# Kernel optimization log

Hardware: AMD Instinct MI355X
Metric: run time of the kernel (lower is better)

## Reference

```python
import jax, jax.numpy as jnp
import numpy as np

N, E = 50000, 300000
IN, FC, AC, H, C1, C2, OUT = 1024, 128, 20, 4, 10, 5, 3
FCN = FC + AC + H * C2  # 168


def bn_eval(x, g, b):
    # BatchNorm1d in eval mode with running_mean=0, running_var=1
    return x * (g / jnp.sqrt(1.0 + 1e-5)) + b


def add_self_loops(edge_index, edge_attr, n):
    # PyG add_self_loops with fill_value='mean': self-loop attr = mean of incoming edge attrs
    src, dst = edge_index[0], edge_index[1]
    ones = jnp.ones(src.shape[0], jnp.float32)
    deg = jax.ops.segment_sum(ones, dst, num_segments=n)
    mean_attr = jax.ops.segment_sum(edge_attr, dst, num_segments=n) / jnp.maximum(deg, 1.0)[:, None]
    loop = jnp.arange(n, dtype=src.dtype)
    return (jnp.concatenate([src, loop]), jnp.concatenate([dst, loop]),
            jnp.concatenate([edge_attr, mean_attr], 0))


def gatv2(x, src, dst, eattr, Wl, bl, Wr, br, We, att, b, n):
    # GATv2Conv (concat=True, negative_slope=0.2, edge_dim=1)
    h, c = att.shape
    xl = (x @ Wl + bl).reshape(n, h, c)
    xr = (x @ Wr + br).reshape(n, h, c)
    em = (eattr @ We).reshape(-1, h, c)
    m = jax.nn.leaky_relu(xl[src] + xr[dst] + em, 0.2)   # [E', H, C]
    logit = jnp.einsum('ehc,hc->eh', m, att)              # [E', H]
    mx = jax.ops.segment_max(logit, dst, num_segments=n)
    ex = jnp.exp(logit - mx[dst])
    den = jax.ops.segment_sum(ex, dst, num_segments=n)
    alpha = ex / (den[dst] + 1e-16)                       # segment softmax over dst
    out = jax.ops.segment_sum(xl[src] * alpha[..., None], dst, num_segments=n)
    return out.reshape(n, h * c) + b


def setup_inputs() -> dict:
    key = jax.random.key(0)
    ks = jax.random.split(key, 24)
    rn = lambda k, s: jax.random.normal(k, s, jnp.float32) * 0.05
    return {
        'features': jax.random.normal(ks[0], (N, IN), jnp.float32),
        'edges': jax.random.randint(ks[1], (2, E), 0, N),
        'edges2': jax.random.randint(ks[2], (2, E), 0, N),
        'edge_features': jax.random.normal(ks[3], (E, 1), jnp.float32),
        'additional_features': jax.random.normal(ks[4], (N, AC), jnp.float32),
        'sage_Wl': rn(ks[5], (IN, FC)), 'sage_bl': jnp.zeros((FC,), jnp.float32),
        'sage_Wr': rn(ks[6], (IN, FC)),
        'g1_Wl': rn(ks[7], (AC, H * C1)), 'g1_bl': jnp.zeros((H * C1,), jnp.float32),
        'g1_Wr': rn(ks[8], (AC, H * C1)), 'g1_br': jnp.zeros((H * C1,), jnp.float32),
        'g1_We': rn(ks[9], (1, H * C1)), 'g1_att': rn(ks[10], (H, C1)),
        'g1_b': jnp.zeros((H * C1,), jnp.float32),
        'g2_Wl': rn(ks[11], (H * C1, H * C2)), 'g2_bl': jnp.zeros((H * C2,), jnp.float32),
        'g2_Wr': rn(ks[12], (H * C1, H * C2)), 'g2_br': jnp.zeros((H * C2,), jnp.float32),
        'g2_We': rn(ks[13], (1, H * C2)), 'g2_att': rn(ks[14], (H, C2)),
        'g2_b': jnp.zeros((H * C2,), jnp.float32),
        'fc1_W': rn(ks[15], (FCN, FCN)), 'fc1_b': jnp.zeros((FCN,), jnp.float32),
        'fc2_W': rn(ks[16], (FCN, OUT)), 'fc2_b': jnp.zeros((OUT,), jnp.float32),
        'bnx_g': jnp.ones((FC,), jnp.float32), 'bnx_b': jnp.zeros((FC,), jnp.float32),
        'bny_g': jnp.ones((H * C2,), jnp.float32), 'bny_b': jnp.zeros((H * C2,), jnp.float32),
        'bnf_g': jnp.ones((FCN,), jnp.float32), 'bnf_b': jnp.zeros((FCN,), jnp.float32),
    }


def reference(features, edges, edges2, edge_features, additional_features,
              sage_Wl, sage_bl, sage_Wr,
              g1_Wl, g1_bl, g1_Wr, g1_br, g1_We, g1_att, g1_b,
              g2_Wl, g2_bl, g2_Wr, g2_br, g2_We, g2_att, g2_b,
              fc1_W, fc1_b, fc2_W, fc2_b,
              bnx_g, bnx_b, bny_g, bny_b, bnf_g, bnf_b):
    n = features.shape[0]
    # --- SAGEConv (mean aggr): out = lin_l(mean_j x_j) + lin_r(x_i) ---
    src, dst = edges[0], edges[1]
    deg = jax.ops.segment_sum(jnp.ones(src.shape[0], jnp.float32), dst, num_segments=n)
    aggr = jax.ops.segment_sum(features[src], dst, num_segments=n) / jnp.maximum(deg, 1.0)[:, None]
    x = aggr @ sage_Wl + sage_bl + features @ sage_Wr
    x = bn_eval(x, bnx_g, bnx_b)
    # --- GATv2 stack (self loops with mean edge-attr fill) ---
    s2, d2, ea = add_self_loops(edges2, edge_features, n)
    y = gatv2(additional_features, s2, d2, ea, g1_Wl, g1_bl, g1_Wr, g1_br, g1_We, g1_att, g1_b, n)
    y = jax.nn.leaky_relu(y, 0.01)  # activation (dropout off in eval)
    y = gatv2(y, s2, d2, ea, g2_Wl, g2_bl, g2_Wr, g2_br, g2_We, g2_att, g2_b, n)
    y = bn_eval(y, bny_g, bny_b)
    # --- MLP head ---
    z = jax.nn.leaky_relu(jnp.concatenate([x, y], axis=1), 0.01)
    z = jnp.concatenate([z, additional_features], axis=1) @ fc1_W + fc1_b
    z = jax.nn.relu(bn_eval(z, bnf_g, bnf_b))
    return z @ fc2_W + fc2_b
```

## Files before the change

### kernel.cpp

```cpp
#include <hip/hip_runtime.h>
#include <hip/hip_bf16.h>
#include <cfloat>

__device__ __forceinline__ float lrelu(float x, float a) { return x > 0.0f ? x : a * x; }

__device__ __forceinline__ unsigned short f2bf(float f) {
    unsigned u = __float_as_uint(f);
    unsigned r = (u + 0x7FFFu + ((u >> 16) & 1u)) >> 16;
    return (unsigned short)r;
}
__device__ __forceinline__ float bf2f(unsigned short u) {
    return __uint_as_float((unsigned)u << 16);
}

typedef __attribute__((ext_vector_type(8))) short short8;
typedef __attribute__((ext_vector_type(4))) float f32x4;

#define BN_RSQ 0.99999500003749968750f
#define SCAN_B 256
#define BAR_LGKM() asm volatile("s_waitcnt lgkmcnt(0)\n\ts_barrier" ::: "memory")

__global__ void zero_ws(uint4* __restrict__ p, int n16)
{
    int t = blockIdx.x * blockDim.x + threadIdx.x;
    if (t < n16) p[t] = make_uint4(0u, 0u, 0u, 0u);
}

__global__ void prep_all(const float* __restrict__ sWl, const float* __restrict__ sWr,
                         unsigned short* __restrict__ Btp,
                         const float* __restrict__ fc1W, unsigned short* __restrict__ Bt1p,
                         const float* __restrict__ g1Wl, const float* __restrict__ g1Wr,
                         unsigned short* __restrict__ Bg1,
                         const float* __restrict__ g2Wl, const float* __restrict__ g2Wr,
                         unsigned short* __restrict__ Bg2,
                         const int* __restrict__ e1d, const int* __restrict__ e2d,
                         const float* __restrict__ ef,
                         int* __restrict__ cnt1, int* __restrict__ cnt2,
                         float* __restrict__ easum, int E)
{
    int idx = blockIdx.x * blockDim.x + threadIdx.x;
    if (idx < 262144) {
        int j = idx & 7, lane = (idx >> 3) & 63, fn = (idx >> 9) & 3, wid = (idx >> 11) & 3, t = idx >> 13;
        int c = wid * 64 + fn * 16 + (lane & 15);
        int k = t * 32 + (lane >> 4) * 8 + j;
        float v = (c < 128) ? sWl[(size_t)k * 128 + c] : sWr[(size_t)k * 128 + (c - 128)];
        Btp[idx] = f2bf(v);
        return;
    }
    idx -= 262144;
    if (idx < 36864) {
        int j = idx & 7, lane = (idx >> 3) & 63, fn = (idx >> 9) & 3, q = idx >> 11;
        int wid = q % 3, t = q / 3;
        int c = wid * 64 + fn * 16 + (lane & 15);
        int k = t * 32 + (lane >> 4) * 8 + j;
        float v = (c < 168 && k < 168) ? fc1W[(size_t)k * 168 + c] : 0.0f;
        Bt1p[idx] = f2bf(v);
        return;
    }
    idx -= 36864;
    if (idx < 2560) {
        int j = idx & 7, lane = (idx >> 3) & 63, fn = idx >> 9;
        int c = fn * 16 + (lane & 15);
        int k = (lane >> 4) * 8 + j;
        float v = 0.0f;
        if (k < 20) v = (c < 40) ? g1Wl[(size_t)k * 40 + c] : g1Wr[(size_t)k * 40 + (c - 40)];
        Bg1[idx] = f2bf(v);
        return;
    }
    idx -= 2560;
    if (idx < 3072) {
        int j = idx & 7, lane = (idx >> 3) & 63, q = idx >> 9;
        int fn = q % 3, t = q / 3;
        int c = fn * 16 + (lane & 15);
        int k = t * 32 + (lane >> 4) * 8 + j;
        float v = 0.0f;
        if (k < 40 && c < 40) v = (c < 20) ? g2Wl[(size_t)k * 20 + c] : g2Wr[(size_t)k * 20 + (c - 20)];
        Bg2[idx] = f2bf(v);
        return;
    }
    idx -= 3072;
    if (idx < E) {
        atomicAdd(&cnt1[e1d[idx]], 1);
        int d2 = e2d[idx];
        atomicAdd(&cnt2[d2], 1);
        atomicAdd(&easum[d2], ef[idx]);
    }
}

__global__ void scan1(const int* __restrict__ cnt1, const int* __restrict__ cnt2,
                      int* __restrict__ off1, int* __restrict__ off2,
                      int* __restrict__ bsum1, int* __restrict__ bsum2, int M)
{
    __shared__ int sh[SCAN_B];
    int y = blockIdx.y;
    const int* cnt = y ? cnt2 : cnt1;
    int* excl = y ? off2 : off1;
    int* bsum = y ? bsum2 : bsum1;
    int i = blockIdx.x * SCAN_B + threadIdx.x;
    int v = (i < M) ? cnt[i] + y : 0;
    sh[threadIdx.x] = v;
    __syncthreads();
    for (int o = 1; o < SCAN_B; o <<= 1) {
        int t = (threadIdx.x >= o) ? sh[threadIdx.x - o] : 0;
        __syncthreads();
        sh[threadIdx.x] += t;
        __syncthreads();
    }
    if (i < M) excl[i] = sh[threadIdx.x] - v;
    if (threadIdx.x == SCAN_B - 1) bsum[blockIdx.x] = sh[threadIdx.x];
}

__global__ void scan2(int* __restrict__ bsum1, int* __restrict__ bsum2, int nb)
{
    __shared__ int sh[SCAN_B];
    int* bsum = blockIdx.y ? bsum2 : bsum1;
    int v = ((int)threadIdx.x < nb) ? bsum[threadIdx.x] : 0;
    sh[threadIdx.x] = v;
    __syncthreads();
    for (int o = 1; o < SCAN_B; o <<= 1) {
        int t = (threadIdx.x >= o) ? sh[threadIdx.x - o] : 0;
        __syncthreads();
        sh[threadIdx.x] += t;
        __syncthreads();
    }
    if ((int)threadIdx.x < nb) bsum[threadIdx.x] = sh[threadIdx.x] - v;
}

__global__ void scan3(int* __restrict__ off1, int* __restrict__ off2,
                      const int* __restrict__ bsum1, const int* __restrict__ bsum2,
                      const int* __restrict__ cnt1, const int* __restrict__ cnt2,
                      const float* __restrict__ easum, float* __restrict__ ealoop, int M)
{
    int y = blockIdx.y;
    int* off = y ? off2 : off1;
    const int* bsum = y ? bsum2 : bsum1;
    const int* cnt = y ? cnt2 : cnt1;
    int i = blockIdx.x * SCAN_B + threadIdx.x;
    if (i < M) {
        int v = off[i] + bsum[blockIdx.x];
        off[i] = v;
        if (i == M - 1) off[M] = v + cnt[i] + y;
        if (y) ealoop[i] = easum[i] / fmaxf((float)cnt2[i], 1.0f);
    }
}

__global__ __launch_bounds__(256) void stageA(
    const float* __restrict__ A, const unsigned short* __restrict__ Btp,
    unsigned short* __restrict__ P,
    const int* __restrict__ e1s, const int* __restrict__ e1d,
    const int* __restrict__ e2s, const int* __restrict__ e2d,
    const float* __restrict__ ef, const float* __restrict__ ealoop,
    const int* __restrict__ off1, const int* __restrict__ off2,
    int* __restrict__ cnt1, int* __restrict__ cnt2,
    int* __restrict__ srcs1, int2* __restrict__ se2,
    const float* __restrict__ addf, const unsigned short* __restrict__ Bg1,
    const float* __restrict__ g1bl, const float* __restrict__ g1br,
    unsigned short* __restrict__ xl1b, unsigned short* __restrict__ xr1b,
    int M, int E, int Eext, int Gg, int Gf)
{
    __shared__ __align__(16) char smem[20480];
    const int bid = blockIdx.x;
    const int tid = threadIdx.x;

    if (bid < Gg) {
        typedef unsigned short As2_t[64][72];
        As2_t* As2 = reinterpret_cast<As2_t*>(smem);
        const int wid = tid >> 6, lane = tid & 63;
        const int m0 = bid * 64;
        const int l16 = lane & 15, g = lane >> 4;
        const int colbase = wid * 64 + l16;
        const short8* Bv = reinterpret_cast<const short8*>(Btp);
        const int srow = tid >> 4, scol = (tid & 15) * 4;

        f32x4 acc[4][4] = {};
        float4 rcur[4], rnext[4];

#pragma unroll
        for (int p = 0; p < 4; ++p) {
            int ar = m0 + p * 16 + srow;
            rcur[p] = make_float4(0.f, 0.f, 0.f, 0.f);
            if (ar < M) rcur[p] = *reinterpret_cast<const float4*>(&A[(size_t)ar * 1024 + scol]);
        }
#pragma unroll
        for (int p = 0; p < 4; ++p) {
            ushort4 u;
            u.x = f2bf(rcur[p].x); u.y = f2bf(rcur[p].y); u.z = f2bf(rcur[p].z); u.w = f2bf(rcur[p].w);
            *reinterpret_cast<ushort4*>(&As2[0][p * 16 + srow][scol]) = u;
        }
#pragma unroll
        for (int p = 0; p < 4; ++p) {
            int ar = m0 + p * 16 + srow;
            rcur[p] = make_float4(0.f, 0.f, 0.f, 0.f);
            if (ar < M) rcur[p] = *reinterpret_cast<const float4*>(&A[(size_t)ar * 1024 + 64 + scol]);
        }
        BAR_LGKM();

        for (int c = 0; c < 16; ++c) {
            const int buf = c & 1;
            short8 bfr[2][4];
#pragma unroll
            for (int t = 0; t < 2; ++t)
#pragma unroll
                for (int fn = 0; fn < 4; ++fn)
                    bfr[t][fn] = Bv[(((c * 2 + t) * 4 + wid) * 4 + fn) * 64 + lane];
            if (c < 14) {
                const int k0 = (c + 2) * 64;
#pragma unroll
                for (int p = 0; p < 4; ++p) {
                    int ar = m0 + p * 16 + srow;
                    rnext[p] = make_float4(0.f, 0.f, 0.f, 0.f);
                    if (ar < M) rnext[p] = *reinterpret_cast<const float4*>(&A[(size_t)ar * 1024 + k0 + scol]);
                }
            }
#pragma unroll
            for (int t = 0; t < 2; ++t) {
                short8 afr[4];
#pragma unroll
                for (int fm = 0; fm < 4; ++fm)
                    afr[fm] = *reinterpret_cast<const short8*>(&As2[buf][fm * 16 + l16][t * 32 + g * 8]);
#pragma unroll
                for (int fm = 0; fm < 4; ++fm)
#pragma unroll
                    for (int fn = 0; fn < 4; ++fn)
                        acc[fm][fn] = __builtin_amdgcn_mfma_f32_16x16x32_bf16(
                            afr[fm], bfr[t][fn], acc[fm][fn], 0, 0, 0);
            }
            if (c < 15) {
#pragma unroll
                for (int p = 0; p < 4; ++p) {
                    ushort4 u;
                    u.x = f2bf(rcur[p].x); u.y = f2bf(rcur[p].y);
                    u.z = f2bf(rcur[p].z); u.w = f2bf(rcur[p].w);
                    *reinterpret_cast<ushort4*>(&As2[buf ^ 1][p * 16 + srow][scol]) = u;
                }
            }
            BAR_LGKM();
#pragma unroll
            for (int p = 0; p < 4; ++p) rcur[p] = rnext[p];
        }

#pragma unroll
        for (int fm = 0; fm < 4; ++fm) {
#pragma unroll
            for (int r = 0; r < 4; ++r) {
                int row = m0 + fm * 16 + g * 4 + r;
                if (row < M) {
#pragma unroll
                    for (int fn = 0; fn < 4; ++fn)
                        P[(size_t)row * 256 + colbase + fn * 16] = f2bf(acc[fm][fn][r]);
                }
            }
        }
    } else if (bid < Gg + Gf) {
        int t = (bid - Gg) * 256 + tid;
        if (t < E) {
            int d = e1d[t];
            int pos = atomicSub(&cnt1[d], 1) - 1;
            srcs1[off1[d] + pos] = e1s[t];
        }
        int t2 = t - E;
        if (t2 >= 0 && t2 < Eext) {
            if (t2 < E) {
                int d = e2d[t2];
                int pos = atomicSub(&cnt2[d], 1) - 1;
                se2[off2[d] + pos] = make_int2(e2s[t2], __float_as_int(ef[t2]));
            } else {
                int nn = t2 - E;
                se2[off2[nn + 1] - 1] = make_int2(nn, __float_as_int(ealoop[nn]));
            }
        }
    } else {
        const int wid = tid >> 6, lane = tid & 63;
        const int tile = (bid - Gg - Gf) * 4 + wid;
        const int m0 = tile * 64;
        if (m0 >= M) return;
        unsigned short (*xs)[40] = reinterpret_cast<unsigned short(*)[40]>(smem + wid * 5120);
        const int l16 = lane & 15, g = lane >> 4;
        const short8* Bv = reinterpret_cast<const short8*>(Bg1);

#pragma unroll
        for (int i = 0; i < 5; ++i) {
            int q = i * 64 + lane;
            int f = q * 4;
            int row = f / 20, col = f % 20;
            int ar = m0 + row;
            float4 v = make_float4(0.f, 0.f, 0.f, 0.f);
            if (ar < M) v = *reinterpret_cast<const float4*>(&addf[(size_t)ar * 20 + col]);
            ushort4 u;
            u.x = f2bf(v.x); u.y = f2bf(v.y); u.z = f2bf(v.z); u.w = f2bf(v.w);
            *reinterpret_cast<ushort4*>(&xs[row][col]) = u;
        }
        ushort4 zz; zz.x = 0; zz.y = 0; zz.z = 0; zz.w = 0;
#pragma unroll
        for (int c = 20; c < 32; c += 4)
            *reinterpret_cast<ushort4*>(&xs[lane][c]) = zz;

        f32x4 acc[4][5] = {};
        short8 afr[4], bfr[5];
#pragma unroll
        for (int fm = 0; fm < 4; ++fm)
            afr[fm] = *reinterpret_cast<const short8*>(&xs[fm * 16 + l16][g * 8]);
#pragma unroll
        for (int fn = 0; fn < 5; ++fn)
            bfr[fn] = Bv[fn * 64 + lane];
#pragma unroll
        for (int fm = 0; fm < 4; ++fm)
#pragma unroll
            for (int fn = 0; fn < 5; ++fn)
                acc[fm][fn] = __builtin_amdgcn_mfma_f32_16x16x32_bf16(
                    afr[fm], bfr[fn], acc[fm][fn], 0, 0, 0);

#pragma unroll
        for (int fm = 0; fm < 4; ++fm) {
#pragma unroll
            for (int r = 0; r < 4; ++r) {
                int row = m0 + fm * 16 + g * 4 + r;
                if (row < M) {
#pragma unroll
                    for (int fn = 0; fn < 5; ++fn) {
                        int col = fn * 16 + l16;
                        float v = acc[fm][fn][r];
                        if (col < 40) {
                            int h = col / 10, c = col % 10;
                            xl1b[((size_t)row * 4 + h) * 16 + c] = f2bf(v + g1bl[col]);
                        } else if (col < 80) {
                            int cc = col - 40, h = cc / 10, c = cc % 10;
                            xr1b[((size_t)row * 4 + h) * 16 + c] = f2bf(v + g1br[cc]);
                        }
                    }
                }
            }
        }
    }
}

template <int H, int C, int BPAD>
__device__ __forceinline__ void gat_node_compute(
    const int2* __restrict__ se2, const int* __restrict__ off2,
    const unsigned short* __restrict__ xlb, const unsigned short* __restrict__ xrb,
    const float* __restrict__ We, const float* __restrict__ att,
    int n, int h, float* __restrict__ outc)
{
    float xrc[C], atth[C], weh[C];
    {
        short8 sv[BPAD / 8];
#pragma unroll
        for (int q = 0; q < BPAD / 8; ++q)
            sv[q] = *reinterpret_cast<const short8*>(&xrb[((size_t)n * H + h) * BPAD + q * 8]);
#pragma unroll
        for (int c = 0; c < C; ++c) xrc[c] = bf2f((unsigned short)sv[c / 8][c % 8]);
    }
#pragma unroll
    for (int c = 0; c < C; ++c) {
        atth[c] = att[h * C + c];
        weh[c]  = We[h * C + c];
    }

    const int beg = off2[n], end = off2[n + 1];
    float mx = -FLT_MAX, den = 0.0f;
    float accv[C] = {};
    for (int j = beg; j < end; ++j) {
        int2 se = se2[j];
        int s = se.x;
        float ea = __int_as_float(se.y);
        short8 sv[BPAD / 8];
#pragma unroll
        for (int q = 0; q < BPAD / 8; ++q)
            sv[q] = *reinterpret_cast<const short8*>(&xlb[((size_t)s * H + h) * BPAD + q * 8]);
        float xv[C];
        float lg = 0.0f;
#pragma unroll
        for (int c = 0; c < C; ++c) {
            xv[c] = bf2f((unsigned short)sv[c / 8][c % 8]);
            float m = xv[c] + xrc[c] + ea * weh[c];
            lg += lrelu(m, 0.2f) * atth[c];
        }
        if (lg > mx) {
            float sc = __expf(mx - lg);
            den *= sc;
#pragma unroll
            for (int c = 0; c < C; ++c) accv[c] *= sc;
            mx = lg;
        }
        float ex = __expf(lg - mx);
        den += ex;
#pragma unroll
        for (int c = 0; c < C; ++c) accv[c] += ex * xv[c];
    }
    float inv = 1.0f / (den + 1e-16f);
#pragma unroll
    for (int c = 0; c < C; ++c) outc[c] = accv[c] * inv;
}

__global__ void stageB(const int* __restrict__ srcs1, const int* __restrict__ off1,
                       const unsigned short* __restrict__ P, const float* __restrict__ bl,
                       const float* __restrict__ bng, const float* __restrict__ bnb,
                       unsigned short* __restrict__ z128,
                       const int2* __restrict__ se2, const int* __restrict__ off2,
                       const unsigned short* __restrict__ xl1b, const unsigned short* __restrict__ xr1b,
                       const float* __restrict__ g1We, const float* __restrict__ g1att,
                       const float* __restrict__ g1b, float* __restrict__ y1,
                       int N, int Gg)
{
    const int bid = blockIdx.x;
    if (bid < Gg) {
        int t = bid * 256 + threadIdx.x;
        if (t >= N * 16) return;
        int n = t >> 4, g = t & 15;
        int beg = off1[n], end = off1[n + 1];
        float a[8] = {};
        for (int j = beg; j < end; ++j) {
            int s = srcs1[j];
            short8 v = *reinterpret_cast<const short8*>(&P[(size_t)s * 256 + g * 8]);
#pragma unroll
            for (int k = 0; k < 8; ++k) a[k] += bf2f((unsigned short)v[k]);
        }
        float inv = 1.0f / fmaxf((float)(end - beg), 1.0f);
        short8 pr = *reinterpret_cast<const short8*>(&P[(size_t)n * 256 + 128 + g * 8]);
        short8 zo;
#pragma unroll
        for (int k = 0; k < 8; ++k) {
            int cc = g * 8 + k;
            float x = a[k] * inv + bl[cc] + bf2f((unsigned short)pr[k]);
            x = x * (bng[cc] * BN_RSQ) + bnb[cc];
            zo[k] = (short)f2bf(lrelu(x, 0.01f));
        }
        *reinterpret_cast<short8*>(&z128[(size_t)n * 128 + g * 8]) = zo;
    } else {
        int t = (bid - Gg) * 256 + threadIdx.x;
        if (t >= N * 4) return;
        int n = t >> 2, h = t & 3;
        float oc[10];
        gat_node_compute<4, 10, 16>(se2, off2, xl1b, xr1b, g1We, g1att, n, h, oc);
#pragma unroll
        for (int c = 0; c < 10; ++c) {
            int jch = h * 10 + c;
            y1[(size_t)n * 40 + jch] = lrelu(oc[c] + g1b[jch], 0.01f);
        }
    }
}

__global__ __launch_bounds__(64) void gat_lin2_mfma(
    const float* __restrict__ X, const unsigned short* __restrict__ Bp,
    const float* __restrict__ bl, const float* __restrict__ br,
    unsigned short* __restrict__ xlb, unsigned short* __restrict__ xrb, int M)
{
    __shared__ unsigned short xs[64][72];
    const int lane = threadIdx.x;
    const int m0 = blockIdx.x * 64;
    const int l16 = lane & 15, g = lane >> 4;
    const short8* Bv = reinterpret_cast<const short8*>(Bp);

#pragma unroll
    for (int i = 0; i < 10; ++i) {
        int q = i * 64 + lane;
        int f = q * 4;
        int row = f / 40, col = f % 40;
        int ar = m0 + row;
        float4 v = make_float4(0.f, 0.f, 0.f, 0.f);
        if (ar < M) v = *reinterpret_cast<const float4*>(&X[(size_t)ar * 40 + col]);
        ushort4 u;
        u.x = f2bf(v.x); u.y = f2bf(v.y); u.z = f2bf(v.z); u.w = f2bf(v.w);
        *reinterpret_cast<ushort4*>(&xs[row][col]) = u;
    }
    ushort4 zz; zz.x = 0; zz.y = 0; zz.z = 0; zz.w = 0;
#pragma unroll
    for (int c = 40; c < 64; c += 4)
        *reinterpret_cast<ushort4*>(&xs[lane][c]) = zz;

    f32x4 acc[4][3] = {};
#pragma unroll
    for (int t = 0; t < 2; ++t) {
        short8 afr[4], bfr[3];
#pragma unroll
        for (int fm = 0; fm < 4; ++fm)
            afr[fm] = *reinterpret_cast<const short8*>(&xs[fm * 16 + l16][t * 32 + g * 8]);
#pragma unroll
        for (int fn = 0; fn < 3; ++fn)
            bfr[fn] = Bv[(t * 3 + fn) * 64 + lane];
#pragma unroll
        for (int fm = 0; fm < 4; ++fm)
#pragma unroll
            for (int fn = 0; fn < 3; ++fn)
                acc[fm][fn] = __builtin_amdgcn_mfma_f32_16x16x32_bf16(
                    afr[fm], bfr[fn], acc[fm][fn], 0, 0, 0);
    }

#pragma unroll
    for (int fm = 0; fm < 4; ++fm) {
#pragma unroll
        for (int r = 0; r < 4; ++r) {
            int row = m0 + fm * 16 + g * 4 + r;
            if (row < M) {
#pragma unroll
                for (int fn = 0; fn < 3; ++fn) {
                    int col = fn * 16 + l16;
                    float v = acc[fm][fn][r];
                    if (col < 20) {
                        int h = col / 5, c = col % 5;
                        xlb[((size_t)row * 4 + h) * 8 + c] = f2bf(v + bl[col]);
                    } else if (col < 40) {
                        int cc = col - 20, h = cc / 5, c = cc % 5;
                        xrb[((size_t)row * 4 + h) * 8 + c] = f2bf(v + br[cc]);
                    }
                }
            }
        }
    }
}

__global__ __launch_bounds__(256) void mlp_mfma(
    const unsigned short* __restrict__ z128, const float* __restrict__ addf,
    const int2* __restrict__ se2, const int* __restrict__ off2,
    const unsigned short* __restrict__ xl2b, const unsigned short* __restrict__ xr2b,
    const float* __restrict__ g2We, const float* __restrict__ g2att,
    const float* __restrict__ g2b,
    const float* __restrict__ bnyg, const float* __restrict__ bnyb,
    const unsigned short* __restrict__ Bt1p,
    const float* __restrict__ fc1b, const float* __restrict__ bnfg, const float* __restrict__ bnfb,
    const float* __restrict__ fc2W, const float* __restrict__ fc2b,
    float* __restrict__ out, int M)
{
    __shared__ __align__(16) char smem[64 * 169 * 4];
    unsigned short (*zs)[200] = reinterpret_cast<unsigned short(*)[200]>(smem);
    float (*ts)[169] = reinterpret_cast<float(*)[169]>(smem);
    const int tid = threadIdx.x;
    const int wid = tid >> 6, lane = tid & 63;
    const int m0 = blockIdx.x * 64;
    const int l16 = lane & 15, g = lane >> 4;
    const short8* Bv = reinterpret_cast<const short8*>(Bt1p);

    {
        int row = tid >> 2, h = tid & 3;
        int n = m0 + row;
        if (n < M) {
            float oc[5];
            gat_node_compute<4, 5, 8>(se2, off2, xl2b, xr2b, g2We, g2att, n, h, oc);
#pragma unroll
            for (int c = 0; c < 5; ++c) {
                int jch = h * 5 + c;
                float v = oc[c] + g2b[jch];
                v = v * (bnyg[jch] * BN_RSQ) + bnyb[jch];
                zs[row][128 + jch] = f2bf(lrelu(v, 0.01f));
            }
        } else {
#pragma unroll
            for (int c = 0; c < 5; ++c) zs[row][128 + h * 5 + c] = 0;
        }
    }

#pragma unroll
    for (int p = 0; p < 13; ++p) {
        int idx = p * 256 + tid;
        if (idx < 3200) {
            int row = idx / 50, c4 = (idx % 50) * 4;
            if (c4 >= 128 && c4 < 148) continue;
            int ar = m0 + row;
            ushort4 u; u.x = 0; u.y = 0; u.z = 0; u.w = 0;
            if (ar < M) {
                if (c4 < 128) {
                    u = *reinterpret_cast<const ushort4*>(&z128[(size_t)ar * 128 + c4]);
                } else if (c4 >= 148 && c4 < 168) {
                    float4 v = *reinterpret_cast<const float4*>(&addf[(size_t)ar * 20 + (c4 - 148)]);
                    u.x = f2bf(v.x); u.y = f2bf(v.y); u.z = f2bf(v.z); u.w = f2bf(v.w);
                }
            }
            *reinterpret_cast<ushort4*>(&zs[row][c4]) = u;
        }
    }
    __syncthreads();

    f32x4 acc[4][4] = {};
    if (wid < 3) {
#pragma unroll
        for (int t = 0; t < 6; ++t) {
            short8 afr[4], bfr[4];
#pragma unroll
            for (int fm = 0; fm < 4; ++fm)
                afr[fm] = *reinterpret_cast<const short8*>(&zs[fm * 16 + l16][t * 32 + g * 8]);
#pragma unroll
            for (int fn = 0; fn < 4; ++fn)
                bfr[fn] = Bv[((t * 3 + wid) * 4 + fn) * 64 + lane];
#pragma unroll
            for (int fm = 0; fm < 4; ++fm)
#pragma unroll
                for (int fn = 0; fn < 4; ++fn)
                    acc[fm][fn] = __builtin_amdgcn_mfma_f32_16x16x32_bf16(
                        afr[fm], bfr[fn], acc[fm][fn], 0, 0, 0);
        }
    }
    __syncthreads();
    if (wid < 3) {
        const int colbase = wid * 64 + l16;
#pragma unroll
        for (int fm = 0; fm < 4; ++fm) {
#pragma unroll
            for (int r = 0; r < 4; ++r) {
                int rr = fm * 16 + g * 4 + r;
#pragma unroll
                for (int fn = 0; fn < 4; ++fn) {
                    int col = colbase + fn * 16;
                    if (col < 168) {
                        float v = acc[fm][fn][r] + fc1b[col];
                        v = v * (bnfg[col] * BN_RSQ) + bnfb[col];
                        ts[rr][col] = fmaxf(v, 0.0f);
                    }
                }
            }
        }
    }
    __syncthreads();
    if (tid < 192) {
        int r = tid & 63, c = tid >> 6;
        float acc2 = fc2b[c];
#pragma unroll 4
        for (int k = 0; k < 168; ++k) acc2 += ts[r][k] * fc2W[k * 3 + c];
        int row = m0 + r;
        if (row < M) out[(size_t)row * 3 + c] = acc2;
    }
}

extern "C" void kernel_launch(void* const* d_in, const int* in_sizes, int n_in,
                              void* d_out, int out_size, void* d_ws, size_t ws_size,
                              hipStream_t stream)
{
    const float* features = (const float*)d_in[0];
    const int*   e1       = (const int*)d_in[1];
    const int*   e2       = (const int*)d_in[2];
    const float* ef       = (const float*)d_in[3];
    const float* addf     = (const float*)d_in[4];
    const float* sage_Wl  = (const float*)d_in[5];
    const float* sage_bl  = (const float*)d_in[6];
    const float* sage_Wr  = (const float*)d_in[7];
    const float* g1_Wl = (const float*)d_in[8];
    const float* g1_bl = (const float*)d_in[9];
    const float* g1_Wr = (const float*)d_in[10];
    const float* g1_br = (const float*)d_in[11];
    const float* g1_We = (const float*)d_in[12];
    const float* g1_att = (const float*)d_in[13];
    const float* g1_b = (const float*)d_in[14];
    const float* g2_Wl = (const float*)d_in[15];
    const float* g2_bl = (const float*)d_in[16];
    const float* g2_Wr = (const float*)d_in[17];
    const float* g2_br = (const float*)d_in[18];
    const float* g2_We = (const float*)d_in[19];
    const float* g2_att = (const float*)d_in[20];
    const float* g2_b = (const float*)d_in[21];
    const float* fc1_W = (const float*)d_in[22];
    const float* fc1_b = (const float*)d_in[23];
    const float* fc2_W = (const float*)d_in[24];
    const float* fc2_b = (const float*)d_in[25];
    const float* bnx_g = (const float*)d_in[26];
    const float* bnx_b = (const float*)d_in[27];
    const float* bny_g = (const float*)d_in[28];
    const float* bny_b = (const float*)d_in[29];
    const float* bnf_g = (const float*)d_in[30];
    const float* bnf_b = (const float*)d_in[31];

    const int N = in_sizes[0] / 1024;
    const int E = in_sizes[3];
    const int Eext = E + N;
    const int* e1s = e1, *e1d = e1 + E;
    const int* e2s = e2, *e2d = e2 + E;
    const int nb = (N + SCAN_B - 1) / SCAN_B;

    char* wb = (char*)d_ws;
    size_t off = 0;
    auto takeB = [&](size_t bytes) { char* p = wb + off; off = (off + bytes + 255) & ~(size_t)255; return p; };
    unsigned short* P = (unsigned short*)takeB((size_t)N * 256 * 2);
    unsigned short* z128 = (unsigned short*)takeB((size_t)N * 128 * 2);
    float* ealoop = (float*)takeB((size_t)N * 4);
    unsigned short* xl1b = (unsigned short*)takeB((size_t)N * 64 * 2);
    unsigned short* xr1b = (unsigned short*)takeB((size_t)N * 64 * 2);
    float* y1 = (float*)takeB((size_t)N * 40 * 4);
    unsigned short* xl2b = (unsigned short*)takeB((size_t)N * 32 * 2);
    unsigned short* xr2b = (unsigned short*)takeB((size_t)N * 32 * 2);
    unsigned short* Btp  = (unsigned short*)takeB((size_t)256 * 1024 * 2);
    unsigned short* Bt1p = (unsigned short*)takeB((size_t)36864 * 2);
    unsigned short* Bg1  = (unsigned short*)takeB((size_t)2560 * 2);
    unsigned short* Bg2  = (unsigned short*)takeB((size_t)3072 * 2);
    char* zero_beg = wb + off;
    int* cnt1    = (int*)takeB((size_t)N * 4);
    int* cnt2    = (int*)takeB((size_t)N * 4);
    float* easum = (float*)takeB((size_t)N * 4);
    size_t zero_len = (size_t)((wb + off) - zero_beg);
    int* off1  = (int*)takeB((size_t)(N + 1) * 4);
    int* off2  = (int*)takeB((size_t)(N + 1) * 4);
    int* bsum1 = (int*)takeB(SCAN_B * 4);
    int* bsum2 = (int*)takeB(SCAN_B * 4);
    int* srcs1 = (int*)takeB((size_t)E * 4);
    int2* se2  = (int2*)takeB((size_t)Eext * 8);

    const int B = 256;
    const int n16 = (int)(zero_len / 16);
    zero_ws<<<(n16 + B - 1) / B, B, 0, stream>>>((uint4*)zero_beg, n16);

    const int prep_total = 262144 + 36864 + 2560 + 3072 + E;
    prep_all<<<(prep_total + B - 1) / B, B, 0, stream>>>(
        sage_Wl, sage_Wr, Btp, fc1_W, Bt1p,
        g1_Wl, g1_Wr, Bg1, g2_Wl, g2_Wr, Bg2,
        e1d, e2d, ef, cnt1, cnt2, easum, E);

    scan1<<<dim3(nb, 2), SCAN_B, 0, stream>>>(cnt1, cnt2, off1, off2, bsum1, bsum2, N);
    scan2<<<dim3(1, 2), SCAN_B, 0, stream>>>(bsum1, bsum2, nb);
    scan3<<<dim3(nb, 2), SCAN_B, 0, stream>>>(off1, off2, bsum1, bsum2, cnt1, cnt2,
                                              easum, ealoop, N);

    const int mtiles = (N + 63) / 64;
    const int Gf = (E + Eext + B - 1) / B;
    const int Gl = (mtiles + 3) / 4;
    stageA<<<mtiles + Gf + Gl, 256, 0, stream>>>(
        features, Btp, P,
        e1s, e1d, e2s, e2d, ef, ealoop, off1, off2, cnt1, cnt2, srcs1, se2,
        addf, Bg1, g1_bl, g1_br, xl1b, xr1b,
        N, E, Eext, mtiles, Gf);

    const int Gg = (N * 16 + B - 1) / B;
    const int Gn = (N * 4 + B - 1) / B;
    stageB<<<Gg + Gn, 256, 0, stream>>>(
        srcs1, off1, P, sage_bl, bnx_g, bnx_b, z128,
        se2, off2, xl1b, xr1b, g1_We, g1_att, g1_b, y1, N, Gg);

    gat_lin2_mfma<<<mtiles, 64, 0, stream>>>(y1, Bg2, g2_bl, g2_br, xl2b, xr2b, N);

    mlp_mfma<<<mtiles, 256, 0, stream>>>(
        z128, addf, se2, off2, xl2b, xr2b, g2_We, g2_att, g2_b, bny_g, bny_b,
        Bt1p, fc1_b, bnf_g, bnf_b, fc2_W, fc2_b, (float*)d_out, N);
}
```

Baseline: 258.8 us.

## Fuse GATv2 layer-2 linear into stageB and prefetch B fragments in GEMM

The first GATv2 aggregation in stageB now writes its 64-node tile of activations as bf16 into shared memory. Three waves of the same block then run the layer-2 linear projection with MFMA there, which removes the separate gat_lin2_mfma launch and the fp32 y1 round trip through global memory. The SAGE GEMM in stageA also double-buffers its B-operand register fragments so the next chunk loads while the current MFMAs run. The cost is more register pressure in the GEMM and some idle waves during the small fused MFMA phase.

Measured after the change: 249.5 us (median of 2 runs). 3.6% less time.

```diff
diff --git a/kernel.cpp b/kernel.cpp
--- a/kernel.cpp
+++ b/kernel.cpp
@@ -174,6 +174,7 @@
 
         f32x4 acc[4][4] = {};
         float4 rcur[4], rnext[4];
+        short8 bcur[2][4], bnext[2][4];
 
 #pragma unroll
         for (int p = 0; p < 4; ++p) {
@@ -182,6 +183,11 @@
             if (ar < M) rcur[p] = *reinterpret_cast<const float4*>(&A[(size_t)ar * 1024 + scol]);
         }
 #pragma unroll
+        for (int t = 0; t < 2; ++t)
+#pragma unroll
+            for (int fn = 0; fn < 4; ++fn)
+                bcur[t][fn] = Bv[((t * 4 + wid) * 4 + fn) * 64 + lane];
+#pragma unroll
         for (int p = 0; p < 4; ++p) {
             ushort4 u;
             u.x = f2bf(rcur[p].x); u.y = f2bf(rcur[p].y); u.z = f2bf(rcur[p].z); u.w = f2bf(rcur[p].w);
@@ -197,12 +203,13 @@
 
         for (int c = 0; c < 16; ++c) {
             const int buf = c & 1;
-            short8 bfr[2][4];
-#pragma unroll
-            for (int t = 0; t < 2; ++t)
-#pragma unroll
-                for (int fn = 0; fn < 4; ++fn)
-                    bfr[t][fn] = Bv[(((c * 2 + t) * 4 + wid) * 4 + fn) * 64 + lane];
+            if (c < 15) {
+#pragma unroll
+                for (int t = 0; t < 2; ++t)
+#pragma unroll
+                    for (int fn = 0; fn < 4; ++fn)
+                        bnext[t][fn] = Bv[((((c + 1) * 2 + t) * 4 + wid) * 4 + fn) * 64 + lane];
+            }
             if (c < 14) {
                 const int k0 = (c + 2) * 64;
 #pragma unroll
@@ -223,7 +230,7 @@
 #pragma unroll
                     for (int fn = 0; fn < 4; ++fn)
                         acc[fm][fn] = __builtin_amdgcn_mfma_f32_16x16x32_bf16(
-                            afr[fm], bfr[t][fn], acc[fm][fn], 0, 0, 0);
+                            afr[fm], bcur[t][fn], acc[fm][fn], 0, 0, 0);
             }
             if (c < 15) {
 #pragma unroll
@@ -237,6 +244,10 @@
             BAR_LGKM();
 #pragma unroll
             for (int p = 0; p < 4; ++p) rcur[p] = rnext[p];
+#pragma unroll
+            for (int t = 0; t < 2; ++t)
+#pragma unroll
+                for (int fn = 0; fn < 4; ++fn) bcur[t][fn] = bnext[t][fn];
         }
 
 #pragma unroll
@@ -392,19 +403,25 @@
     for (int c = 0; c < C; ++c) outc[c] = accv[c] * inv;
 }
 
-__global__ void stageB(const int* __restrict__ srcs1, const int* __restrict__ off1,
-                       const unsigned short* __restrict__ P, const float* __restrict__ bl,
-                       const float* __restrict__ bng, const float* __restrict__ bnb,
-                       unsigned short* __restrict__ z128,
-                       const int2* __restrict__ se2, const int* __restrict__ off2,
-                       const unsigned short* __restrict__ xl1b, const unsigned short* __restrict__ xr1b,
-                       const float* __restrict__ g1We, const float* __restrict__ g1att,
-                       const float* __restrict__ g1b, float* __restrict__ y1,
-                       int N, int Gg)
-{
+__global__ __launch_bounds__(256) void stageB(
+    const int* __restrict__ srcs1, const int* __restrict__ off1,
+    const unsigned short* __restrict__ P, const float* __restrict__ bl,
+    const float* __restrict__ bng, const float* __restrict__ bnb,
+    unsigned short* __restrict__ z128,
+    const int2* __restrict__ se2, const int* __restrict__ off2,
+    const unsigned short* __restrict__ xl1b, const unsigned short* __restrict__ xr1b,
+    const float* __restrict__ g1We, const float* __restrict__ g1att,
+    const float* __restrict__ g1b,
+    const unsigned short* __restrict__ Bg2,
+    const float* __restrict__ g2bl, const float* __restrict__ g2br,
+    unsigned short* __restrict__ xl2b, unsigned short* __restrict__ xr2b,
+    int N, int Gg)
+{
+    __shared__ unsigned short xs[64][72];
     const int bid = blockIdx.x;
+    const int tid = threadIdx.x;
     if (bid < Gg) {
-        int t = bid * 256 + threadIdx.x;
+        int t = bid * 256 + tid;
         if (t >= N * 16) return;
         int n = t >> 4, g = t & 15;
         int beg = off1[n], end = off1[n + 1];
@@ -427,81 +444,57 @@
         }
         *reinterpret_cast<short8*>(&z128[(size_t)n * 128 + g * 8]) = zo;
     } else {
-        int t = (bid - Gg) * 256 + threadIdx.x;
-        if (t >= N * 4) return;
-        int n = t >> 2, h = t & 3;
-        float oc[10];
-        gat_node_compute<4, 10, 16>(se2, off2, xl1b, xr1b, g1We, g1att, n, h, oc);
-#pragma unroll
-        for (int c = 0; c < 10; ++c) {
-            int jch = h * 10 + c;
-            y1[(size_t)n * 40 + jch] = lrelu(oc[c] + g1b[jch], 0.01f);
-        }
-    }
-}
-
-__global__ __launch_bounds__(64) void gat_lin2_mfma(
-    const float* __restrict__ X, const unsigned short* __restrict__ Bp,
-    const float* __restrict__ bl, const float* __restrict__ br,
-    unsigned short* __restrict__ xlb, unsigned short* __restrict__ xrb, int M)
-{
-    __shared__ unsigned short xs[64][72];
-    const int lane = threadIdx.x;
-    const int m0 = blockIdx.x * 64;
-    const int l16 = lane & 15, g = lane >> 4;
-    const short8* Bv = reinterpret_cast<const short8*>(Bp);
-
-#pragma unroll
-    for (int i = 0; i < 10; ++i) {
-        int q = i * 64 + lane;
-        int f = q * 4;
-        int row = f / 40, col = f % 40;
-        int ar = m0 + row;
-        float4 v = make_float4(0.f, 0.f, 0.f, 0.f);
-        if (ar < M) v = *reinterpret_cast<const float4*>(&X[(size_t)ar * 40 + col]);
-        ushort4 u;
-        u.x = f2bf(v.x); u.y = f2bf(v.y); u.z = f2bf(v.z); u.w = f2bf(v.w);
-        *reinterpret_cast<ushort4*>(&xs[row][col]) = u;
-    }
-    ushort4 zz; zz.x = 0; zz.y = 0; zz.z = 0; zz.w = 0;
-#pragma unroll
-    for (int c = 40; c < 64; c += 4)
-        *reinterpret_cast<ushort4*>(&xs[lane][c]) = zz;
-
-    f32x4 acc[4][3] = {};
-#pragma unroll
-    for (int t = 0; t < 2; ++t) {
-        short8 afr[4], bfr[3];
-#pragma unroll
-        for (int fm = 0; fm < 4; ++fm)
-            afr[fm] = *reinterpret_cast<const short8*>(&xs[fm * 16 + l16][t * 32 + g * 8]);
-#pragma unroll
-        for (int fn = 0; fn < 3; ++fn)
-            bfr[fn] = Bv[(t * 3 + fn) * 64 + lane];
-#pragma unroll
-        for (int fm = 0; fm < 4; ++fm)
-#pragma unroll
-            for (int fn = 0; fn < 3; ++fn)
-                acc[fm][fn] = __builtin_amdgcn_mfma_f32_16x16x32_bf16(
-                    afr[fm], bfr[fn], acc[fm][fn], 0, 0, 0);
-    }
-
-#pragma unroll
-    for (int fm = 0; fm < 4; ++fm) {
-#pragma unroll
-        for (int r = 0; r < 4; ++r) {
-            int row = m0 + fm * 16 + g * 4 + r;
-            if (row < M) {
-#pragma unroll
-                for (int fn = 0; fn < 3; ++fn) {
-                    int col = fn * 16 + l16;
-                    float v = acc[fm][fn][r];
-                    if (col < 20) {
-                        int h = col / 5, c = col % 5;
-                        xlb[((size_t)row * 4 + h) * 8 + c] = f2bf(v + bl[col]);
-                    } else if (col < 40) {
-                        int cc = col - 20, h = cc / 5, c = cc % 5;
-                        xrb[((size_t)row * 4 + h) * 8 + c] = f2bf(v + br[cc]);
+        const int m0 = (bid - Gg) * 64;
+        ushort4 zz; zz.x = 0; zz.y = 0; zz.z = 0; zz.w = 0;
+#pragma unroll
+        for (int i = 0; i < 5; ++i) {
+            int idx = i * 256 + tid;
+            if (idx < 1152) reinterpret_cast<ushort4*>(&xs[0][0])[idx] = zz;
+        }
+        __syncthreads();
+        {
+            int row = tid >> 2, h = tid & 3;
+            int n = m0 + row;
+            if (n < N) {
+                float oc[10];
+                gat_node_compute<4, 10, 16>(se2, off2, xl1b, xr1b, g1We, g1att, n, h, oc);
+#pragma unroll
+                for (int c = 0; c < 10; ++c) {
+                    int jch = h * 10 + c;
+                    xs[row][jch] = f2bf(lrelu(oc[c] + g1b[jch], 0.01f));
+                }
+            }
+        }
+        __syncthreads();
+        const int wid = tid >> 6, lane = tid & 63;
+        const int l16 = lane & 15, g = lane >> 4;
+        if (wid < 3) {
+            const short8* Bv = reinterpret_cast<const short8*>(Bg2);
+            f32x4 acc[4] = {};
+#pragma unroll
+            for (int t = 0; t < 2; ++t) {
+                short8 bfr = Bv[(t * 3 + wid) * 64 + lane];
+#pragma unroll
+                for (int fm = 0; fm < 4; ++fm) {
+                    short8 afr = *reinterpret_cast<const short8*>(&xs[fm * 16 + l16][t * 32 + g * 8]);
+                    acc[fm] = __builtin_amdgcn_mfma_f32_16x16x32_bf16(afr, bfr, acc[fm], 0, 0, 0);
+                }
+            }
+#pragma unroll
+            for (int fm = 0; fm < 4; ++fm) {
+#pragma unroll
+                for (int r = 0; r < 4; ++r) {
+                    int row = m0 + fm * 16 + g * 4 + r;
+                    if (row < N) {
+                        int col = wid * 16 + l16;
+                        float v = acc[fm][r];
+                        if (col < 20) {
+                            int h = col / 5, c = col % 5;
+                            xl2b[((size_t)row * 4 + h) * 8 + c] = f2bf(v + g2bl[col]);
+                        } else if (col < 40) {
+                            int cc = col - 20, h = cc / 5, c = cc % 5;
+                            xr2b[((size_t)row * 4 + h) * 8 + c] = f2bf(v + g2br[cc]);
+                        }
                     }
                 }
             }
@@ -672,7 +665,6 @@
     float* ealoop = (float*)takeB((size_t)N * 4);
     unsigned short* xl1b = (unsigned short*)takeB((size_t)N * 64 * 2);
     unsigned short* xr1b = (unsigned short*)takeB((size_t)N * 64 * 2);
-    float* y1 = (float*)takeB((size_t)N * 40 * 4);
     unsigned short* xl2b = (unsigned short*)takeB((size_t)N * 32 * 2);
     unsigned short* xr2b = (unsigned short*)takeB((size_t)N * 32 * 2);
     unsigned short* Btp  = (unsigned short*)takeB((size_t)256 * 1024 * 2);
@@ -719,9 +711,8 @@
     const int Gn = (N * 4 + B - 1) / B;
     stageB<<<Gg + Gn, 256, 0, stream>>>(
         srcs1, off1, P, sage_bl, bnx_g, bnx_b, z128,
-        se2, off2, xl1b, xr1b, g1_We, g1_att, g1_b, y1, N, Gg);
-
-    gat_lin2_mfma<<<mtiles, 64, 0, stream>>>(y1, Bg2, g2_bl, g2_br, xl2b, xr2b, N);
+        se2, off2, xl1b, xr1b, g1_We, g1_att, g1_b,
+        Bg2, g2_bl, g2_br, xl2b, xr2b, N, Gg);
 
     mlp_mfma<<<mtiles, 256, 0, stream>>>(
         z128, addf, se2, off2, xl2b, xr2b, g2_We, g2_att, g2_b, bny_g, bny_b,
```
